# Performance work log

Measured on AMD Instinct MI355X. Metric: run time of the kernel, lower is better.

Reference implementation:

```python
import jax, jax.numpy as jnp
import numpy as np

EPS_BN = 1e-3  # nn.BatchNorm1d(num_channels, eps=0.001)
B, C, N = 16, 256, 2048
NUM_SA = 4


def _bn(x, g, b, m, v):
    # eval-mode BatchNorm1d over channel dim of [B, C, N]
    return g[:, None] * (x - m[:, None]) * jax.lax.rsqrt(v[:, None] + EPS_BN) + b[:, None]


def _sa_layer(x, qk_w, v_w, v_b, t_w, t_b, g, b, m, var):
    # q_conv and k_conv share weights -> energy = (Wx)^T (Wx)
    q = jnp.einsum('oc,bcn->bon', qk_w, x)              # [B, C//4, N]
    energy = jnp.einsum('bcm,bcn->bmn', q, q)           # [B, N, N]
    attn = jax.nn.softmax(energy, axis=-1)
    # offset-attention: extra column-sum normalization (dim=1)
    attn = attn / (1e-9 + attn.sum(axis=1, keepdims=True))
    xv = jnp.einsum('oc,bcn->bon', v_w, x) + v_b[:, None]   # [B, C, N]
    x_r = jnp.einsum('bcn,bnm->bcm', xv, attn)              # bmm(x_v, attention)
    t = jnp.einsum('oc,bcn->bon', t_w, x - x_r) + t_b[:, None]
    return x + jax.nn.relu(_bn(t, g, b, m, var))


def setup_inputs() -> dict:
    key = jax.random.key(0)
    ks = jax.random.split(key, 24)
    f32 = jnp.float32
    d = {}
    d['x'] = jax.random.normal(ks[0], (B, C, N), dtype=f32)
    d['conv1_w'] = jax.random.normal(ks[1], (C, C), dtype=f32) * 0.05
    d['conv2_w'] = jax.random.normal(ks[2], (C, C), dtype=f32) * 0.05
    for i, nm in enumerate(['bn1', 'bn2']):
        kk = jax.random.split(ks[3 + i], 4)
        d[nm + '_g'] = 1.0 + 0.05 * jax.random.normal(kk[0], (C,), dtype=f32)
        d[nm + '_b'] = 0.05 * jax.random.normal(kk[1], (C,), dtype=f32)
        d[nm + '_m'] = 0.05 * jax.random.normal(kk[2], (C,), dtype=f32)
        d[nm + '_v'] = jax.random.uniform(kk[3], (C,), dtype=f32, minval=0.5, maxval=1.5)
    d['sa_qk_w'] = jax.random.normal(ks[5], (NUM_SA, C // 4, C), dtype=f32) * 0.05
    d['sa_v_w'] = jax.random.normal(ks[6], (NUM_SA, C, C), dtype=f32) * 0.05
    d['sa_v_b'] = jax.random.normal(ks[7], (NUM_SA, C), dtype=f32) * 0.05
    d['sa_t_w'] = jax.random.normal(ks[8], (NUM_SA, C, C), dtype=f32) * 0.05
    d['sa_t_b'] = jax.random.normal(ks[9], (NUM_SA, C), dtype=f32) * 0.05
    d['sa_g'] = 1.0 + 0.05 * jax.random.normal(ks[10], (NUM_SA, C), dtype=f32)
    d['sa_b'] = 0.05 * jax.random.normal(ks[11], (NUM_SA, C), dtype=f32)
    d['sa_m'] = 0.05 * jax.random.normal(ks[12], (NUM_SA, C), dtype=f32)
    d['sa_var'] = jax.random.uniform(ks[13], (NUM_SA, C), dtype=f32, minval=0.5, maxval=1.5)
    d['flag'] = 0  # False -> primary bn branch
    return d


def reference(x, conv1_w, conv2_w, bn1_g, bn1_b, bn1_m, bn1_v,
              bn2_g, bn2_b, bn2_m, bn2_v,
              sa_qk_w, sa_v_w, sa_v_b, sa_t_w, sa_t_b,
              sa_g, sa_b, sa_m, sa_var, flag):
    h = jax.nn.relu(_bn(jnp.einsum('oc,bcn->bon', conv1_w, x), bn1_g, bn1_b, bn1_m, bn1_v))
    h = jax.nn.relu(_bn(jnp.einsum('oc,bcn->bon', conv2_w, h), bn2_g, bn2_b, bn2_m, bn2_v))
    outs = []
    for i in range(NUM_SA):
        h = _sa_layer(h, sa_qk_w[i], sa_v_w[i], sa_v_b[i], sa_t_w[i], sa_t_b[i],
                      sa_g[i], sa_b[i], sa_m[i], sa_var[i])
        outs.append(h)
    return jnp.concatenate(outs, axis=1)  # [B, 4*C, N]
```

## Files before the change

kernel.cpp:

```cpp
#include <hip/hip_runtime.h>
#include <hip/hip_bf16.h>
#include <hip/hip_fp16.h>

static constexpr int Bn = 16;
static constexpr int Cc = 256;
static constexpr int Nn = 2048;
static constexpr int C4 = 64;
static constexpr float LOG2E = 1.4426950408889634f;

typedef _Float16 half_t;
typedef __attribute__((ext_vector_type(8))) _Float16 half8;
typedef __attribute__((ext_vector_type(4))) _Float16 half4;
typedef __attribute__((ext_vector_type(8))) short short8;
typedef __attribute__((ext_vector_type(4))) float float4v;

static constexpr long sNC = (long)Nn * Cc;
static constexpr long sNQ = (long)Nn * C4;

#define DEVI __device__ __forceinline__

DEVI float bf2f(unsigned short u) { return __uint_as_float(((unsigned)u) << 16); }
DEVI unsigned short f2bf(float f) {
    unsigned x = __float_as_uint(f);
    x += 0x7fffu + ((x >> 16) & 1u);
    return (unsigned short)(x >> 16);
}

DEVI void gload16(const void* g, void* l) {
    __builtin_amdgcn_global_load_lds(
        (const __attribute__((address_space(1))) unsigned int*)g,
        (__attribute__((address_space(3))) unsigned int*)l, 16, 0, 0);
}

enum { EPI_RAW = 0, EPI_H = 1, EPI_XV = 2 };

template<int MODE, int BM, int BN, int WI, int WJ, bool BF16OUT>
__global__ __launch_bounds__(WI * WJ * 64)
void mgemm(const half_t* __restrict__ A, long aB,
           const half_t* __restrict__ Bm, long bB,
           void* __restrict__ Yv, long yB, int ldy,
           const float* __restrict__ bias,
           const float* __restrict__ bng, const float* __restrict__ bnb,
           const float* __restrict__ bnm, const float* __restrict__ bnv,
           int K)
{
    constexpr int NW = WI * WJ;
    __shared__ __align__(16) half_t Als[2][BM][32];
    __shared__ __align__(16) half_t Bls[2][BN][32];

    const int tid  = threadIdx.x;
    const int w    = tid >> 6;
    const int lane = tid & 63;
    const int wi   = w % WI;
    const int wj   = w / WI;
    const int quad = lane >> 4, m16 = lane & 15;
    const int lr   = lane >> 2, lc = lane & 3;
    const int b    = blockIdx.z;
    const int j0   = blockIdx.x * BN;
    const int i0   = blockIdx.y * BM;

    const half_t* Ab = A + (size_t)b * aB;
    const half_t* Bb = Bm + (size_t)b * bB;

    float4v acc[4][4];
    #pragma unroll
    for (int i = 0; i < 4; ++i)
        #pragma unroll
        for (int j = 0; j < 4; ++j) acc[i][j] = (float4v)0.f;

    for (int k0 = 0; k0 < K; k0 += 64) {
        #pragma unroll
        for (int s = 0; s < 2; ++s) {
            const int kk = k0 + s * 32 + lc * 8;
            #pragma unroll
            for (int t = 0; t < BM / (16 * NW); ++t) {
                const int row = (t * NW + w) * 16;
                gload16(Ab + (size_t)(i0 + row + lr) * K + kk, &Als[s][row][0]);
            }
            #pragma unroll
            for (int t = 0; t < BN / (16 * NW); ++t) {
                const int row = (t * NW + w) * 16;
                gload16(Bb + (size_t)(j0 + row + lr) * K + kk, &Bls[s][row][0]);
            }
        }
        __syncthreads();
        #pragma unroll
        for (int s = 0; s < 2; ++s) {
            half8 af[4], bf[4];
            #pragma unroll
            for (int t = 0; t < 4; ++t)
                af[t] = *(const half8*)&Als[s][wi * 64 + t * 16 + m16][quad * 8];
            #pragma unroll
            for (int t = 0; t < 4; ++t)
                bf[t] = *(const half8*)&Bls[s][wj * 64 + t * 16 + m16][quad * 8];
            #pragma unroll
            for (int ti = 0; ti < 4; ++ti)
                #pragma unroll
                for (int tj = 0; tj < 4; ++tj)
                    acc[ti][tj] = __builtin_amdgcn_mfma_f32_16x16x32_f16(
                        af[ti], bf[tj], acc[ti][tj], 0, 0, 0);
        }
        __syncthreads();
    }

    #pragma unroll
    for (int ti = 0; ti < 4; ++ti) {
        const int il = i0 + wi * 64 + ti * 16 + quad * 4;
        #pragma unroll
        for (int tj = 0; tj < 4; ++tj) {
            const int jl = j0 + wj * 64 + tj * 16 + m16;
            float4v v = acc[ti][tj];
            if (MODE == EPI_RAW) {
                half4 o;
                #pragma unroll
                for (int r = 0; r < 4; ++r) o[r] = (half_t)v[r];
                *(half4*)((half_t*)Yv + (size_t)b * yB + (size_t)jl * ldy + il) = o;
            } else if (MODE == EPI_H) {
                half4 o;
                #pragma unroll
                for (int r = 0; r < 4; ++r) {
                    const float sc = bng[il + r] * rsqrtf(bnv[il + r] + 1e-3f);
                    const float sh = bnb[il + r] - bnm[il + r] * sc;
                    o[r] = (half_t)fmaxf(fmaf(v[r], sc, sh), 0.f);
                }
                *(half4*)((half_t*)Yv + (size_t)b * yB + (size_t)jl * ldy + il) = o;
            } else {
                const float bj = bias[jl];
                if (BF16OUT) {
                    ushort4 o;
                    o.x = f2bf(v[0] + bj); o.y = f2bf(v[1] + bj);
                    o.z = f2bf(v[2] + bj); o.w = f2bf(v[3] + bj);
                    *(ushort4*)((unsigned short*)Yv + (size_t)b * yB + (size_t)jl * ldy + il) = o;
                } else {
                    half4 o;
                    #pragma unroll
                    for (int r = 0; r < 4; ++r) o[r] = (half_t)(v[r] + bj);
                    *(half4*)((half_t*)Yv + (size_t)b * yB + (size_t)jl * ldy + il) = o;
                }
            }
        }
    }
}

__global__ __launch_bounds__(256)
void estats(const half_t* __restrict__ q, float* __restrict__ Pbuf)
{
    __shared__ __align__(16) half_t sA[128 * 64];
    __shared__ __align__(16) half_t sB[128 * 64];
    __shared__ float red[2][2][4][16][2];
    const int tid = threadIdx.x, w = tid >> 6, lane = tid & 63;
    const int wi = w & 1, wj = w >> 1, quad = lane >> 4, m16 = lane & 15;
    const int b = blockIdx.z, j0 = blockIdx.x * 128, i0 = blockIdx.y * 128;
    const half_t* qb = q + (size_t)b * sNQ;

    #pragma unroll
    for (int t = 0; t < 4; ++t) {
        const int g = w * 256 + t * 64 + lane;
        const int r = g >> 3, c = g & 7;
        const int cs = c ^ (r & 7);
        gload16(qb + (size_t)(i0 + r) * 64 + cs * 8, sA + (w * 256 + t * 64) * 8);
        gload16(qb + (size_t)(j0 + r) * 64 + cs * 8, sB + (w * 256 + t * 64) * 8);
    }
    __syncthreads();

    half8 an[4][2], bm[4][2];
    #pragma unroll
    for (int t = 0; t < 4; ++t)
        #pragma unroll
        for (int ks = 0; ks < 2; ++ks) {
            const int pc = ((ks * 4 + quad) ^ (m16 & 7)) * 8;
            an[t][ks] = *(const half8*)&sA[(wi * 64 + t * 16 + m16) * 64 + pc];
            bm[t][ks] = *(const half8*)&sB[(wj * 64 + t * 16 + m16) * 64 + pc];
        }

    #pragma unroll
    for (int tj = 0; tj < 4; ++tj) {
        float4v e[4];
        #pragma unroll
        for (int ti = 0; ti < 4; ++ti) {
            e[ti] = (float4v)0.f;
            e[ti] = __builtin_amdgcn_mfma_f32_16x16x32_f16(an[ti][0], bm[tj][0], e[ti], 0, 0, 0);
            e[ti] = __builtin_amdgcn_mfma_f32_16x16x32_f16(an[ti][1], bm[tj][1], e[ti], 0, 0, 0);
        }
        float lmax = -1e30f;
        #pragma unroll
        for (int ti = 0; ti < 4; ++ti)
            #pragma unroll
            for (int r = 0; r < 4; ++r) lmax = fmaxf(lmax, e[ti][r]);
        lmax = fmaxf(lmax, __shfl_xor(lmax, 16));
        lmax = fmaxf(lmax, __shfl_xor(lmax, 32));
        float ls = 0.f;
        #pragma unroll
        for (int ti = 0; ti < 4; ++ti)
            #pragma unroll
            for (int r = 0; r < 4; ++r) ls += __expf(e[ti][r] - lmax);
        ls += __shfl_xor(ls, 16);
        ls += __shfl_xor(ls, 32);
        if (quad == 0) { red[wi][wj][tj][m16][0] = lmax; red[wi][wj][tj][m16][1] = ls; }
    }
    __syncthreads();
    if (tid < 128) {
        const int wj2 = tid >> 6, tj2 = (tid >> 4) & 3, mm = tid & 15;
        const float m0 = red[0][wj2][tj2][mm][0], s0 = red[0][wj2][tj2][mm][1];
        const float m1 = red[1][wj2][tj2][mm][0], s1 = red[1][wj2][tj2][mm][1];
        const float M = fmaxf(m0, m1);
        const float S = s0 * __expf(m0 - M) + s1 * __expf(m1 - M);
        const int m = j0 + wj2 * 64 + tj2 * 16 + mm;
        *(float2*)(Pbuf + (((size_t)b * Nn + m) * 16 + blockIdx.y) * 2) = make_float2(M, S);
    }
}

__global__ __launch_bounds__(1024)
void flashxr(const half_t* __restrict__ q, const half_t* __restrict__ xv,
             const half_t* __restrict__ h, const float* __restrict__ Pbuf,
             const half_t* __restrict__ tw, const float* __restrict__ tb,
             const float* __restrict__ bng, const float* __restrict__ bnb,
             const float* __restrict__ bnm, const float* __restrict__ bnv,
             float* __restrict__ outL, half_t* __restrict__ hNext)
{
    __shared__ __align__(16) half_t sQ[2][128 * 64];
    __shared__ __align__(16) half_t sXV[256 * 128];
    __shared__ __align__(16) half_t sP[128 * 128];
    __shared__ float sOff[Nn];

    const int tid = threadIdx.x, w = tid >> 6, lane = tid & 63;
    const int quad = lane >> 4, m16 = lane & 15;
    const int wiE = w & 1, wjE = w >> 1;
    const int wi = w & 3, wj = w >> 2;
    const int wiT = w & 1, wjT = w >> 1;
    const int f = blockIdx.x;
    const int W = (f & 7) * 32 + (f >> 3);
    const int b = W >> 4, j0 = (W & 15) * 128;
    const half_t* qb  = q + (size_t)b * sNQ;
    const half_t* xvb = xv + (size_t)b * sNC;

    const int sr = tid >> 3, sc = tid & 7;
    const int qsw = (sc ^ (sr & 7)) * 8;

    gload16(qb + (size_t)(j0 + sr) * 64 + qsw, sP + (size_t)tid * 8);
    gload16(qb + (size_t)sr * 64 + qsw,        &sQ[0][(size_t)tid * 8]);

    {
        const float* pB = Pbuf + (size_t)b * Nn * 32;
        for (int i = tid; i < Nn; i += 1024) {
            const float4v* p4 = (const float4v*)(pB + (size_t)i * 32);
            float4v v[8];
            #pragma unroll
            for (int t = 0; t < 8; ++t) v[t] = p4[t];
            float M = -1e30f;
            #pragma unroll
            for (int t = 0; t < 8; ++t) { M = fmaxf(M, v[t][0]); M = fmaxf(M, v[t][2]); }
            float S = 0.f;
            #pragma unroll
            for (int t = 0; t < 8; ++t) {
                S += v[t][1] * __expf(v[t][0] - M);
                S += v[t][3] * __expf(v[t][2] - M);
            }
            sOff[i] = fmaf(M, LOG2E, __log2f(S));
        }
    }
    __syncthreads();
    half8 bq[2];
    #pragma unroll
    for (int ks = 0; ks < 2; ++ks)
        bq[ks] = *(const half8*)&sP[(wjE * 16 + m16) * 64
                                    + (((ks * 4 + quad) ^ (m16 & 7)) * 8)];
    __syncthreads();

    float4v acc[4][2];
    #pragma unroll
    for (int i = 0; i < 4; ++i)
        #pragma unroll
        for (int j = 0; j < 2; ++j) acc[i][j] = (float4v)0.f;
    float csa = 0.f;

    for (int nc = 0; nc < 16; ++nc) {
        const int cur = nc & 1;
        #pragma unroll
        for (int t = 0; t < 4; ++t) {
            const int g = t * 1024 + tid;
            const int r = g >> 4, c = g & 15;
            gload16(xvb + (size_t)r * Nn + nc * 128 + ((c ^ (r & 15)) * 8),
                    sXV + (size_t)g * 8);
        }
        if (nc < 15)
            gload16(qb + (size_t)((nc + 1) * 128 + sr) * 64 + qsw,
                    &sQ[cur ^ 1][(size_t)tid * 8]);

        const int nbase = nc * 128 + wiE * 64 + quad * 4;
        #pragma unroll
        for (int ti = 0; ti < 4; ++ti) {
            const int arow = (wiE * 64 + ti * 16 + m16) * 64;
            const half8 an0 = *(const half8*)&sQ[cur][arow + ((quad ^ (m16 & 7)) * 8)];
            const half8 an1 = *(const half8*)&sQ[cur][arow + (((4 + quad) ^ (m16 & 7)) * 8)];
            float4v e = (float4v)0.f;
            e = __builtin_amdgcn_mfma_f32_16x16x32_f16(an0, bq[0], e, 0, 0, 0);
            e = __builtin_amdgcn_mfma_f32_16x16x32_f16(an1, bq[1], e, 0, 0, 0);
            const float4v o4 = *(const float4v*)&sOff[nbase + ti * 16];
            float c0 = 0.f; ushort4 pk;
            #pragma unroll
            for (int r = 0; r < 4; ++r) {
                const float p = __builtin_amdgcn_exp2f(fmaf(e[r], LOG2E, -o4[r]));
                c0 += p; (&pk.x)[r] = f2bf(p);
            }
            csa += c0;
            const int pc  = wiE * 8 + ti * 2 + (quad >> 1);
            const int sub = (quad & 1) * 4;
            const int mrow = wjE * 16 + m16;
            *(ushort4*)&((unsigned short*)sP)[(size_t)mrow * 128 + (pc ^ m16) * 8 + sub] = pk;
        }
        __syncthreads();

        #pragma unroll
        for (int ks = 0; ks < 4; ++ks) {
            short8 xa[4], pb[2];
            #pragma unroll
            for (int ti = 0; ti < 4; ++ti)
                xa[ti] = *(const short8*)&sXV[(wi * 64 + ti * 16 + m16) * 128
                                              + (((ks * 4 + quad) ^ m16) * 8)];
            #pragma unroll
            for (int tj = 0; tj < 2; ++tj)
                pb[tj] = *(const short8*)&sP[(wj * 32 + tj * 16 + m16) * 128
                                             + (((ks * 4 + quad) ^ m16) * 8)];
            #pragma unroll
            for (int ti = 0; ti < 4; ++ti)
                #pragma unroll
                for (int tj = 0; tj < 2; ++tj)
                    acc[ti][tj] = __builtin_amdgcn_mfma_f32_16x16x32_bf16(
                        xa[ti], pb[tj], acc[ti][tj], 0, 0, 0);
        }
        __syncthreads();
    }

    csa += __shfl_xor(csa, 16);
    csa += __shfl_xor(csa, 32);
    float* fb = (float*)sP;
    if (lane < 16) fb[wiE * 128 + wjE * 16 + lane] = csa;
    __syncthreads();
    float csr[2];
    #pragma unroll
    for (int tj = 0; tj < 2; ++tj) {
        const int m = wj * 32 + tj * 16 + m16;
        csr[tj] = 1.0f / (1e-9f + fb[m] + fb[128 + m]);
    }

    const half_t* hb = h + (size_t)b * sNC;
    half_t* sD = sXV;
    #pragma unroll
    for (int ti = 0; ti < 4; ++ti) {
        const int cg = wi * 64 + ti * 16 + quad * 4;
        const int cc = (cg >> 3) ^ (m16 & 7);
        const int sub = (quad & 1) * 4;
        #pragma unroll
        for (int tj = 0; tj < 2; ++tj) {
            const int mr = wj * 32 + tj * 16 + m16;
            const int mg = j0 + mr;
            const half4 hv = *(const half4*)&hb[(size_t)mg * Cc + cg];
            half4 o;
            #pragma unroll
            for (int r = 0; r < 4; ++r)
                o[r] = (half_t)((float)hv[r] - acc[ti][tj][r] * csr[tj]);
            *(half4*)&sD[(size_t)mr * 256 + cc * 8 + sub] = o;
        }
    }
    __syncthreads();

    float4v acc2[4][2];
    #pragma unroll
    for (int i = 0; i < 4; ++i)
        #pragma unroll
        for (int j = 0; j < 2; ++j) acc2[i][j] = (float4v)0.f;
    #pragma unroll
    for (int ks = 0; ks < 8; ++ks) {
        half8 af[4], bf[2];
        #pragma unroll
        for (int tm = 0; tm < 4; ++tm)
            af[tm] = *(const half8*)&sD[(size_t)(wiT * 64 + tm * 16 + m16) * 256
                                        + (((ks * 4 + quad) ^ (m16 & 7)) * 8)];
        #pragma unroll
        for (int tc = 0; tc < 2; ++tc)
            bf[tc] = *(const half8*)&tw[(size_t)(wjT * 32 + tc * 16 + m16) * 256
                                        + ks * 32 + quad * 8];
        #pragma unroll
        for (int tm = 0; tm < 4; ++tm)
            #pragma unroll
            for (int tc = 0; tc < 2; ++tc)
                acc2[tm][tc] = __builtin_amdgcn_mfma_f32_16x16x32_f16(
                    af[tm], bf[tc], acc2[tm][tc], 0, 0, 0);
    }

    const long yB = (long)4 * Cc * Nn;
    float* yb = outL + (size_t)b * yB;
    half_t* hn = hNext ? hNext + (size_t)b * sNC : nullptr;
    #pragma unroll
    for (int tc = 0; tc < 2; ++tc) {
        const int co = wjT * 32 + tc * 16 + m16;
        const float tb2 = tb[co];
        const float sc2 = bng[co] * rsqrtf(bnv[co] + 1e-3f);
        const float sh2 = bnb[co] - bnm[co] * sc2;
        #pragma unroll
        for (int tm = 0; tm < 4; ++tm) {
            const int mg = j0 + wiT * 64 + tm * 16 + quad * 4;
            float4v o;
            #pragma unroll
            for (int r = 0; r < 4; ++r) {
                const float t2  = acc2[tm][tc][r] + tb2;
                const float rel = fmaxf(fmaf(t2, sc2, sh2), 0.f);
                const float hv  = (float)hb[(size_t)(mg + r) * Cc + co];
                const float ov  = hv + rel;
                o[r] = ov;
                if (hn) hn[(size_t)(mg + r) * Cc + co] = (half_t)ov;
            }
            *(float4v*)&yb[(size_t)co * Nn + mg] = o;
        }
    }
}

__global__ __launch_bounds__(256)
void xpose_cast(const float* __restrict__ x, half_t* __restrict__ xT)
{
    __shared__ half_t tile[32][33];
    const int tx = threadIdx.x & 31, ty = threadIdx.x >> 5;
    const int n0 = blockIdx.x * 32, c0 = blockIdx.y * 32, b = blockIdx.z;
    #pragma unroll
    for (int r = 0; r < 4; ++r)
        tile[ty * 4 + r][tx] =
            (half_t)x[((size_t)b * Cc + c0 + ty * 4 + r) * Nn + n0 + tx];
    __syncthreads();
    #pragma unroll
    for (int r = 0; r < 4; ++r)
        xT[((size_t)b * Nn + n0 + ty * 4 + r) * Cc + c0 + tx] = tile[tx][ty * 4 + r];
}

__global__ __launch_bounds__(256)
void castall(const float* __restrict__ c1, const float* __restrict__ c2,
             const float* __restrict__ qk, const float* __restrict__ vw,
             const float* __restrict__ tw, half_t* __restrict__ dst)
{
    const int i = (blockIdx.x * 256 + threadIdx.x) * 4;
    const float* s; int o;
    if      (i < 65536)  { s = c1; o = 0; }
    else if (i < 131072) { s = c2; o = 65536; }
    else if (i < 196608) { s = qk; o = 131072; }
    else if (i < 458752) { s = vw; o = 196608; }
    else                 { s = tw; o = 458752; }
    const float4v v = *(const float4v*)(s + (i - o));
    half4 out;
    #pragma unroll
    for (int r = 0; r < 4; ++r) out[r] = (half_t)v[r];
    *(half4*)(dst + i) = out;
}

extern "C" void kernel_launch(void* const* d_in, const int* in_sizes, int n_in,
                              void* d_out, int out_size, void* d_ws, size_t ws_size,
                              hipStream_t stream)
{
    const float* x    = (const float*)d_in[0];
    const float* c1w  = (const float*)d_in[1];
    const float* c2w  = (const float*)d_in[2];
    const float* bn1g = (const float*)d_in[3], *bn1b = (const float*)d_in[4];
    const float* bn1m = (const float*)d_in[5], *bn1v = (const float*)d_in[6];
    const float* bn2g = (const float*)d_in[7], *bn2b = (const float*)d_in[8];
    const float* bn2m = (const float*)d_in[9], *bn2v = (const float*)d_in[10];
    const float* qkw  = (const float*)d_in[11];
    const float* vw   = (const float*)d_in[12];
    const float* vb   = (const float*)d_in[13];
    const float* tw   = (const float*)d_in[14];
    const float* tb   = (const float*)d_in[15];
    const float* sag  = (const float*)d_in[16];
    const float* sab  = (const float*)d_in[17];
    const float* sam  = (const float*)d_in[18];
    const float* sav  = (const float*)d_in[19];
    float* out = (float*)d_out;

    char* ws = (char*)d_ws;
    const size_t HSZ = (size_t)Bn * Nn * Cc * 2;
    half_t* xT   = (half_t*)(ws);
    half_t* hA   = (half_t*)(ws + HSZ);
    half_t* hBuf = (half_t*)(ws + 2 * HSZ);
    half_t* q_s  = (half_t*)(ws + 3 * HSZ);
    half_t* xv_s = (half_t*)(ws + 3 * HSZ + (size_t)4194304);
    float*  Pbuf = (float*) (ws + 4 * HSZ + (size_t)4194304);
    half_t* warena = (half_t*)(ws + 4 * HSZ + (size_t)8388608);
    half_t* wc1  = warena;
    half_t* wc2  = wc1 + 65536;
    half_t* wqk  = wc2 + 65536;
    half_t* wv   = wqk + 65536;
    half_t* wt   = wv  + 262144;

    dim3 blk(256);

    castall<<<768, blk, 0, stream>>>(c1w, c2w, qkw, vw, tw, warena);
    xpose_cast<<<dim3(Nn / 32, Cc / 32, Bn), blk, 0, stream>>>(x, xT);

    mgemm<EPI_H, 256, 128, 4, 2, false><<<dim3(16, 1, Bn), dim3(512), 0, stream>>>(
        wc1, 0, xT, sNC, hA, sNC, Cc,
        nullptr, bn1g, bn1b, bn1m, bn1v, Cc);
    mgemm<EPI_H, 256, 128, 4, 2, false><<<dim3(16, 1, Bn), dim3(512), 0, stream>>>(
        wc2, 0, hA, sNC, hBuf, sNC, Cc,
        nullptr, bn2g, bn2b, bn2m, bn2v, Cc);

    half_t* hcur = hBuf;
    half_t* hnxt = hA;
    for (int L = 0; L < 4; ++L) {
        mgemm<EPI_RAW, 64, 256, 1, 4, false><<<dim3(8, 1, Bn), blk, 0, stream>>>(
            wqk + (long)L * C4 * Cc, 0, hcur, sNC, q_s, sNQ, C4,
            nullptr, nullptr, nullptr, nullptr, nullptr, Cc);
        estats<<<dim3(16, 16, Bn), blk, 0, stream>>>(q_s, Pbuf);
        mgemm<EPI_XV, 128, 256, 2, 4, true><<<dim3(1, 16, Bn), dim3(512), 0, stream>>>(
            hcur, sNC, wv + (long)L * Cc * Cc, 0, xv_s, (long)Cc * Nn, Nn,
            vb + L * Cc, nullptr, nullptr, nullptr, nullptr, Cc);
        flashxr<<<dim3(256), dim3(1024), 0, stream>>>(
            q_s, xv_s, hcur, Pbuf,
            wt + (long)L * Cc * Cc, tb + L * Cc,
            sag + L * Cc, sab + L * Cc, sam + L * Cc, sav + L * Cc,
            out + (long)L * Cc * Nn, (L < 3) ? hnxt : nullptr);
        half_t* tmp = hcur; hcur = hnxt; hnxt = tmp;
    }
}
```

Before: 714.8 us.

## Double-buffer XV tiles in smaller chunks and read Q directly into registers

The flashxr main loop now processes 64-column chunks instead of 128. The value-projection (XV) tile is double-buffered in LDS, so the next chunk's load overlaps the current chunk's MFMA work. Q fragments are read straight from global memory into registers, which removes the sQ staging buffer and cuts shared memory use. Plain __syncthreads are replaced by a manual lgkmcnt wait plus s_barrier, and setprio raises wave priority around the MFMA bursts. The trade-off is twice as many barriers per pass. There is also a correctness risk if the async global-to-LDS loads are not waited on with vmcnt before the barrier.

```diff
diff --git a/kernel.cpp b/kernel.cpp
--- a/kernel.cpp
+++ b/kernel.cpp
@@ -218,9 +218,8 @@
              const float* __restrict__ bnm, const float* __restrict__ bnv,
              float* __restrict__ outL, half_t* __restrict__ hNext)
 {
-    __shared__ __align__(16) half_t sQ[2][128 * 64];
-    __shared__ __align__(16) half_t sXV[256 * 128];
-    __shared__ __align__(16) half_t sP[128 * 128];
+    __shared__ __align__(16) half_t sXV[2][256 * 64];
+    __shared__ __align__(16) half_t sP[128 * 64];
     __shared__ float sOff[Nn];
 
     const int tid = threadIdx.x, w = tid >> 6, lane = tid & 63;
@@ -234,11 +233,18 @@
     const half_t* qb  = q + (size_t)b * sNQ;
     const half_t* xvb = xv + (size_t)b * sNC;
 
-    const int sr = tid >> 3, sc = tid & 7;
-    const int qsw = (sc ^ (sr & 7)) * 8;
-
-    gload16(qb + (size_t)(j0 + sr) * 64 + qsw, sP + (size_t)tid * 8);
-    gload16(qb + (size_t)sr * 64 + qsw,        &sQ[0][(size_t)tid * 8]);
+    #pragma unroll
+    for (int t = 0; t < 2; ++t) {
+        const int g = t * 1024 + tid;
+        const int r = g >> 3, c = g & 7;
+        gload16(xvb + (size_t)r * Nn + ((c ^ (r & 7)) * 8), &sXV[0][(size_t)g * 8]);
+    }
+    __builtin_amdgcn_sched_barrier(0);
+
+    half8 bq[2];
+    #pragma unroll
+    for (int s = 0; s < 2; ++s)
+        bq[s] = *(const half8*)(qb + (size_t)(j0 + wjE * 16 + m16) * 64 + (s * 4 + quad) * 8);
 
     {
         const float* pB = Pbuf + (size_t)b * Nn * 32;
@@ -259,13 +265,9 @@
             sOff[i] = fmaf(M, LOG2E, __log2f(S));
         }
     }
-    __syncthreads();
-    half8 bq[2];
-    #pragma unroll
-    for (int ks = 0; ks < 2; ++ks)
-        bq[ks] = *(const half8*)&sP[(wjE * 16 + m16) * 64
-                                    + (((ks * 4 + quad) ^ (m16 & 7)) * 8)];
-    __syncthreads();
+    asm volatile("s_waitcnt lgkmcnt(0)" ::: "memory");
+    __builtin_amdgcn_s_barrier();
+    __builtin_amdgcn_sched_barrier(0);
 
     float4v acc[4][2];
     #pragma unroll
@@ -274,29 +276,38 @@
         for (int j = 0; j < 2; ++j) acc[i][j] = (float4v)0.f;
     float csa = 0.f;
 
-    for (int nc = 0; nc < 16; ++nc) {
+    const int mrow = wjE * 16 + m16;
+
+    for (int nc = 0; nc < 32; ++nc) {
         const int cur = nc & 1;
-        #pragma unroll
-        for (int t = 0; t < 4; ++t) {
-            const int g = t * 1024 + tid;
-            const int r = g >> 4, c = g & 15;
-            gload16(xvb + (size_t)r * Nn + nc * 128 + ((c ^ (r & 15)) * 8),
-                    sXV + (size_t)g * 8);
-        }
-        if (nc < 15)
-            gload16(qb + (size_t)((nc + 1) * 128 + sr) * 64 + qsw,
-                    &sQ[cur ^ 1][(size_t)tid * 8]);
-
-        const int nbase = nc * 128 + wiE * 64 + quad * 4;
-        #pragma unroll
-        for (int ti = 0; ti < 4; ++ti) {
-            const int arow = (wiE * 64 + ti * 16 + m16) * 64;
-            const half8 an0 = *(const half8*)&sQ[cur][arow + ((quad ^ (m16 & 7)) * 8)];
-            const half8 an1 = *(const half8*)&sQ[cur][arow + (((4 + quad) ^ (m16 & 7)) * 8)];
+
+        half8 an[2][2];
+        #pragma unroll
+        for (int ti = 0; ti < 2; ++ti)
+            #pragma unroll
+            for (int s = 0; s < 2; ++s)
+                an[ti][s] = *(const half8*)(qb
+                    + (size_t)(nc * 64 + wiE * 32 + ti * 16 + m16) * 64
+                    + (s * 4 + quad) * 8);
+        __builtin_amdgcn_sched_barrier(0);
+
+        if (nc < 31) {
+            #pragma unroll
+            for (int t = 0; t < 2; ++t) {
+                const int g = t * 1024 + tid;
+                const int r = g >> 3, c = g & 7;
+                gload16(xvb + (size_t)r * Nn + (nc + 1) * 64 + ((c ^ (r & 7)) * 8),
+                        &sXV[cur ^ 1][(size_t)g * 8]);
+            }
+        }
+        __builtin_amdgcn_sched_barrier(0);
+
+        #pragma unroll
+        for (int ti = 0; ti < 2; ++ti) {
             float4v e = (float4v)0.f;
-            e = __builtin_amdgcn_mfma_f32_16x16x32_f16(an0, bq[0], e, 0, 0, 0);
-            e = __builtin_amdgcn_mfma_f32_16x16x32_f16(an1, bq[1], e, 0, 0, 0);
-            const float4v o4 = *(const float4v*)&sOff[nbase + ti * 16];
+            e = __builtin_amdgcn_mfma_f32_16x16x32_f16(an[ti][0], bq[0], e, 0, 0, 0);
+            e = __builtin_amdgcn_mfma_f32_16x16x32_f16(an[ti][1], bq[1], e, 0, 0, 0);
+            const float4v o4 = *(const float4v*)&sOff[nc * 64 + wiE * 32 + ti * 16 + quad * 4];
             float c0 = 0.f; ushort4 pk;
             #pragma unroll
             for (int r = 0; r < 4; ++r) {
@@ -304,32 +315,36 @@
                 c0 += p; (&pk.x)[r] = f2bf(p);
             }
             csa += c0;
-            const int pc  = wiE * 8 + ti * 2 + (quad >> 1);
-            const int sub = (quad & 1) * 4;
-            const int mrow = wjE * 16 + m16;
-            *(ushort4*)&((unsigned short*)sP)[(size_t)mrow * 128 + (pc ^ m16) * 8 + sub] = pk;
-        }
-        __syncthreads();
-
-        #pragma unroll
-        for (int ks = 0; ks < 4; ++ks) {
+            const int pc = (wiE * 4 + ti * 2 + (quad >> 1)) ^ (m16 & 7);
+            *(ushort4*)&((unsigned short*)sP)[(size_t)mrow * 64 + pc * 8 + (quad & 1) * 4] = pk;
+        }
+        asm volatile("s_waitcnt lgkmcnt(0)" ::: "memory");
+        __builtin_amdgcn_s_barrier();
+        __builtin_amdgcn_sched_barrier(0);
+
+        #pragma unroll
+        for (int ks = 0; ks < 2; ++ks) {
             short8 xa[4], pb[2];
             #pragma unroll
             for (int ti = 0; ti < 4; ++ti)
-                xa[ti] = *(const short8*)&sXV[(wi * 64 + ti * 16 + m16) * 128
-                                              + (((ks * 4 + quad) ^ m16) * 8)];
+                xa[ti] = *(const short8*)&sXV[cur][(size_t)(wi * 64 + ti * 16 + m16) * 64
+                                                  + (((ks * 4 + quad) ^ (m16 & 7)) * 8)];
             #pragma unroll
             for (int tj = 0; tj < 2; ++tj)
-                pb[tj] = *(const short8*)&sP[(wj * 32 + tj * 16 + m16) * 128
-                                             + (((ks * 4 + quad) ^ m16) * 8)];
+                pb[tj] = *(const short8*)&sP[(size_t)(wj * 32 + tj * 16 + m16) * 64
+                                             + (((ks * 4 + quad) ^ (m16 & 7)) * 8)];
+            __builtin_amdgcn_s_setprio(1);
             #pragma unroll
             for (int ti = 0; ti < 4; ++ti)
                 #pragma unroll
                 for (int tj = 0; tj < 2; ++tj)
                     acc[ti][tj] = __builtin_amdgcn_mfma_f32_16x16x32_bf16(
                         xa[ti], pb[tj], acc[ti][tj], 0, 0, 0);
-        }
-        __syncthreads();
+            __builtin_amdgcn_s_setprio(0);
+        }
+        asm volatile("s_waitcnt lgkmcnt(0)" ::: "memory");
+        __builtin_amdgcn_s_barrier();
+        __builtin_amdgcn_sched_barrier(0);
     }
 
     csa += __shfl_xor(csa, 16);
@@ -345,7 +360,7 @@
     }
 
     const half_t* hb = h + (size_t)b * sNC;
-    half_t* sD = sXV;
+    half_t* sD = &sXV[0][0];
     #pragma unroll
     for (int ti = 0; ti < 4; ++ti) {
         const int cg = wi * 64 + ti * 16 + quad * 4;
```

New measurement: 895.8 us. 1.25x slower.
